# Kernel tuning notes

Hardware: AMD Instinct MI355X
Metric: run time of the kernel (lower is better)

Reference implementation:

```python
import jax, jax.numpy as jnp
import numpy as np
from jax import lax

M = 8   # num_heads
K = 4   # num_points


def conv2d(x, w, b, pad):
    # x: [B,C,H,W], w: [O,I,kh,kw]
    y = lax.conv_general_dilated(x, w, (1, 1), [(pad, pad), (pad, pad)],
                                 dimension_numbers=('NCHW', 'OIHW', 'NCHW'))
    return y + b[None, :, None, None]


def grid_sample_zeros(v, px, py):
    # Bilinear grid_sample, align_corners=True, padding_mode='zeros'.
    # v: [N,Cm,H,W]; px,py: [N,P] in pixel coordinates.
    N, Cm, H, W = v.shape
    x0 = jnp.floor(px); y0 = jnp.floor(py)
    x1 = x0 + 1.0;      y1 = y0 + 1.0
    wx = px - x0;       wy = py - y0
    vflat = v.reshape(N, Cm, H * W)

    def tap(xi, yi):
        valid = (xi >= 0) & (xi <= W - 1) & (yi >= 0) & (yi <= H - 1)
        xc = jnp.clip(xi, 0, W - 1).astype(jnp.int32)
        yc = jnp.clip(yi, 0, H - 1).astype(jnp.int32)
        idx = yc * W + xc                          # [N,P]
        g = jnp.take_along_axis(vflat, idx[:, None, :], axis=2)  # [N,Cm,P]
        return g * valid[:, None, :].astype(v.dtype)

    v00 = tap(x0, y0); v01 = tap(x1, y0)
    v10 = tap(x0, y1); v11 = tap(x1, y1)
    wx = wx[:, None, :]; wy = wy[:, None, :]
    return (v00 * (1 - wx) * (1 - wy) + v01 * wx * (1 - wy)
            + v10 * (1 - wx) * wy + v11 * wx * wy)


def setup_inputs() -> dict:
    key = jax.random.key(0)
    ks = jax.random.split(key, 16)
    B, C, H, W = 8, 256, 64, 64
    s = 0.02
    inp = {
        'f_recalib': jax.random.normal(ks[0], (B, C, H, W), jnp.float32),
        'f_orig':    jax.random.normal(ks[1], (B, C, H, W), jnp.float32),
        'offset_w': jax.random.normal(ks[2], (M * K * 2, C, 3, 3), jnp.float32) * s,
        'offset_b': jnp.zeros((M * K * 2,), jnp.float32),
        'attn_w':   jax.random.normal(ks[3], (M * K, C, 3, 3), jnp.float32) * s,
        'attn_b':   jnp.zeros((M * K,), jnp.float32),
        'value_w':  jax.random.normal(ks[4], (C, C, 1, 1), jnp.float32) * s,
        'value_b':  jnp.zeros((C,), jnp.float32),
        'proj_w':   jax.random.normal(ks[5], (C, C, 1, 1), jnp.float32) * s,
        'proj_b':   jnp.zeros((C,), jnp.float32),
        'mlp_w1':   jax.random.normal(ks[6], (2 * C, C, 1, 1), jnp.float32) * s,
        'mlp_b1':   jnp.zeros((2 * C,), jnp.float32),
        'mlp_w2':   jax.random.normal(ks[7], (C, 2 * C, 1, 1), jnp.float32) * s,
        'mlp_b2':   jnp.zeros((C,), jnp.float32),
    }
    return inp


def reference(f_recalib, f_orig, offset_w, offset_b, attn_w, attn_b,
              value_w, value_b, proj_w, proj_b,
              mlp_w1, mlp_b1, mlp_w2, mlp_b2):
    B, C, H, W = f_recalib.shape
    Cm = C // M

    offsets = conv2d(f_recalib, offset_w, offset_b, 1).reshape(B, M, K, 2, H, W)
    attn = conv2d(f_recalib, attn_w, attn_b, 1).reshape(B, M, K, H, W)
    attn = jax.nn.softmax(attn, axis=2)
    value = conv2d(f_recalib, value_w, value_b, 0)

    gy, gx = jnp.meshgrid(jnp.arange(H, dtype=jnp.float32),
                          jnp.arange(W, dtype=jnp.float32), indexing='ij')
    gx_sym = (W - 1) - gx  # horizontally mirrored x coordinate
    # pixel-space sampling locations (align_corners=True normalization is exactly
    # inverted by grid_sample's unnormalization, so work in pixel coords)
    px = gx_sym[None, None, None] + offsets[:, :, :, 0]  # [B,M,K,H,W]
    py = gy[None, None, None] + offsets[:, :, :, 1]

    v = value.reshape(B * M, Cm, H, W)
    sampled = grid_sample_zeros(v, px.reshape(B * M, -1), py.reshape(B * M, -1))
    sampled = sampled.reshape(B, M, Cm, K, H, W)

    out = (sampled * attn[:, :, None]).sum(axis=3).reshape(B, C, H, W)
    out = conv2d(out, proj_w, proj_b, 0) + f_orig
    h = jax.nn.relu(conv2d(out, mlp_w1, mlp_b1, 0))
    out = conv2d(h, mlp_w2, mlp_b2, 0) + out
    return out
```

## Files before the change

### kernel.cpp

```cpp
#include <hip/hip_runtime.h>
#include <cstddef>

#define P_ 4096
#define PW_ 66

using u16 = unsigned short;
typedef float  f32x4  __attribute__((ext_vector_type(4)));
typedef u16    u16x8  __attribute__((ext_vector_type(8)));
typedef u16    u16x4  __attribute__((ext_vector_type(4)));
typedef __bf16 bf16x8 __attribute__((ext_vector_type(8)));

#define DEVINL __device__ __forceinline__

DEVINL u16 f2bf(float f) {
    union { float f; unsigned u; } v; v.f = f;
    unsigned r = v.u + 0x7fffu + ((v.u >> 16) & 1u);
    return (u16)(r >> 16);
}
DEVINL float bf2f(u16 h) {
    union { unsigned u; float f; } v; v.u = ((unsigned)h) << 16;
    return v.f;
}

DEVINL f32x4 mfma16(u16x8 a, u16x8 b, f32x4 c) {
    return __builtin_amdgcn_mfma_f32_16x16x32_bf16(
        __builtin_bit_cast(bf16x8, a), __builtin_bit_cast(bf16x8, b), c, 0, 0, 0);
}

DEVINL void gload16(const u16* src, const u16* lds_dst) {
    __builtin_amdgcn_global_load_lds(
        (const __attribute__((address_space(1))) void*)src,
        (__attribute__((address_space(3))) void*)lds_dst, 16, 0, 0);
}

__global__ __launch_bounds__(256) void to_nhwc_pad(
    const float* __restrict__ in, u16* __restrict__ xp,
    const float* __restrict__ off_w, const float* __restrict__ attn_w,
    const float* __restrict__ val_w, const float* __restrict__ proj_w,
    const float* __restrict__ w1, const float* __restrict__ w2,
    u16* __restrict__ wbf) {
    const int bx = blockIdx.x, c0 = blockIdx.y * 64, b = blockIdx.z;
    const int t = threadIdx.x;

    if (bx >= 64) {
        const int idx = ((bx - 64) * 32 + blockIdx.y * 8 + b) * 256 + t;
        if (idx >= 614400) return;
        float v;
        if (idx < 221184) {
            int tap = idx / 24576, rem = idx - tap * 24576, oc = rem >> 8, ic = rem & 255;
            v = (oc < 64) ? off_w[(size_t)(oc * 256 + ic) * 9 + tap]
                          : attn_w[(size_t)((oc - 64) * 256 + ic) * 9 + tap];
        } else if (idx < 286720) v = val_w[idx - 221184];
        else if (idx < 352256)   v = proj_w[idx - 286720];
        else if (idx < 483328)   v = w1[idx - 352256];
        else                     v = w2[idx - 483328];
        wbf[idx] = f2bf(v);
        return;
    }

    const int y = bx;
    __shared__ u16 ts[64 * 72];
    const int cl = t >> 4, xq = t & 15;

    if (y == 0) {
        const u16x8 z = (u16x8){0, 0, 0, 0, 0, 0, 0, 0};
        for (int q = t; q < 2080; q += 256) {
            const int p = q >> 3, c8 = q & 7;
            int row, col;
            if (p < 66)       { row = 0;  col = p; }
            else if (p < 132) { row = 65; col = p - 66; }
            else { const int q2 = p - 132; row = 1 + (q2 >> 1); col = (q2 & 1) * 65; }
            *(u16x8*)&xp[((size_t)(b * PW_ + row) * PW_ + col) * 256 + c0 + c8 * 8] = z;
        }
    }

    #pragma unroll
    for (int r = 0; r < 4; ++r) {
        const int c = r * 16 + cl;
        const float4 v = *(const float4*)&in[((size_t)(b * 256 + c0 + c)) * P_ + y * 64 + xq * 4];
        ts[(xq * 4 + 0) * 72 + c] = f2bf(v.x);
        ts[(xq * 4 + 1) * 72 + c] = f2bf(v.y);
        ts[(xq * 4 + 2) * 72 + c] = f2bf(v.z);
        ts[(xq * 4 + 3) * 72 + c] = f2bf(v.w);
    }
    __syncthreads();
    const int px = t >> 2, seg = t & 3;
    u16x8 o0, o1;
    #pragma unroll
    for (int j = 0; j < 8; ++j) {
        o0[j] = ts[px * 72 + seg * 16 + j];
        o1[j] = ts[px * 72 + seg * 16 + 8 + j];
    }
    const size_t base = ((size_t)(b * PW_ + y + 1) * PW_ + 1 + px) * 256 + c0 + seg * 16;
    *(u16x8*)&xp[base]     = o0;
    *(u16x8*)&xp[base + 8] = o1;
}

__global__ __launch_bounds__(256, 2) void conv3x3_mfma(
    const u16* __restrict__ xp, const u16* __restrict__ wconv,
    const u16* __restrict__ wval,
    const float* __restrict__ off_b, const float* __restrict__ attn_b,
    const float* __restrict__ val_b,
    u16* __restrict__ convout, u16* __restrict__ value_bf) {
    const int y = blockIdx.x, b = blockIdx.y;
    const int tid = threadIdx.x, w = tid >> 6, lane = tid & 63, g = lane >> 4, i = lane & 15;
    const int wm = w & 1, wn = w >> 1;
    const int srow = lane >> 4, sc = lane & 15;
    __shared__ u16 lds[40960];

    f32x4 acc[2][3];
    #pragma unroll
    for (int mi = 0; mi < 2; ++mi)
        #pragma unroll
        for (int nj = 0; nj < 3; ++nj) acc[mi][nj] = (f32x4){0.f, 0.f, 0.f, 0.f};
    f32x4 accv[2][8];
    #pragma unroll
    for (int mi = 0; mi < 2; ++mi)
        #pragma unroll
        for (int nj = 0; nj < 8; ++nj) accv[mi][nj] = (f32x4){0.f, 0.f, 0.f, 0.f};

    auto stage = [&](int buf, int c) {
        const int tap = c >> 1, kc = (c & 1) * 128;
        const int dy = tap / 3, dx = tap % 3;
        const u16* xrow = xp + ((size_t)(b * PW_ + y + dy) * PW_ + dx) * 256;
        const u16* wt = wconv + (size_t)(tap * 96) * 256;
        u16* bufA = &lds[buf * 8192];
        u16* bufW = &lds[16384 + buf * 12288];
        #pragma unroll
        for (int t = 0; t < 4; ++t) {
            const int j = w * 4 + t;
            const int row = j * 4 + srow;
            const int cs = sc ^ (row & 7);
            gload16(xrow + (size_t)row * 256 + kc + (cs << 3), &bufA[j * 512]);
        }
        #pragma unroll
        for (int t = 0; t < 6; ++t) {
            const int j = w * 6 + t;
            const int row = j * 4 + srow;
            const int cs = sc ^ (row & 7);
            gload16(wt + (size_t)row * 256 + kc + (cs << 3), &bufW[j * 512]);
        }
    };

    stage(0, 0);
    stage(1, 1);
    asm volatile("s_waitcnt vmcnt(10)" ::: "memory");
    __builtin_amdgcn_s_barrier();

    for (int c = 0; c < 18; ++c) {
        const u16* bufA = &lds[(c & 1) * 8192];
        const u16* bufW = &lds[16384 + (c & 1) * 12288];
        const int kcv = (c & 1) * 128;
        const bool doval = (c == 8) | (c == 9);
        #pragma unroll
        for (int ks = 0; ks < 4; ++ks) {
            u16x8 a[2], bb[3];
            #pragma unroll
            for (int mi = 0; mi < 2; ++mi) {
                const int pr = wm * 32 + mi * 16 + i;
                a[mi] = *(const u16x8*)&bufA[pr * 128 + (((ks * 4 + g) ^ (pr & 7)) << 3)];
            }
            #pragma unroll
            for (int nj = 0; nj < 3; ++nj) {
                const int ocr = wn * 48 + nj * 16 + i;
                bb[nj] = *(const u16x8*)&bufW[ocr * 128 + (((ks * 4 + g) ^ (ocr & 7)) << 3)];
            }
            #pragma unroll
            for (int mi = 0; mi < 2; ++mi)
                #pragma unroll
                for (int nj = 0; nj < 3; ++nj)
                    acc[mi][nj] = mfma16(a[mi], bb[nj], acc[mi][nj]);
            if (doval) {
                #pragma unroll
                for (int nj = 0; nj < 8; ++nj) {
                    const int oc = wn * 128 + nj * 16 + i;
                    const u16x8 bv = *(const u16x8*)&wval[(size_t)oc * 256 + kcv
                                                          + ks * 32 + g * 8];
                    accv[0][nj] = mfma16(a[0], bv, accv[0][nj]);
                    accv[1][nj] = mfma16(a[1], bv, accv[1][nj]);
                }
            }
        }
        __builtin_amdgcn_sched_barrier(0);
        __builtin_amdgcn_s_barrier();
        if (c + 2 < 18) {
            stage(c & 1, c + 2);
            asm volatile("s_waitcnt vmcnt(10)" ::: "memory");
        } else {
            asm volatile("s_waitcnt vmcnt(0)" ::: "memory");
        }
        __builtin_amdgcn_s_barrier();
    }

    #pragma unroll
    for (int mi = 0; mi < 2; ++mi) {
        const int x0 = wm * 32 + mi * 16 + g * 4;
        #pragma unroll
        for (int nj = 0; nj < 3; ++nj) {
            const int oc = wn * 48 + nj * 16 + i;
            const float bv = (oc < 64) ? off_b[oc] : attn_b[oc - 64];
            #pragma unroll
            for (int r = 0; r < 4; ++r)
                convout[((size_t)(b * P_ + y * 64 + x0 + r)) * 96 + oc] =
                    f2bf(acc[mi][nj][r] + bv);
        }
        #pragma unroll
        for (int nj = 0; nj < 8; ++nj) {
            const int oc = wn * 128 + nj * 16 + i;
            const float bv = val_b[oc];
            #pragma unroll
            for (int r = 0; r < 4; ++r)
                value_bf[((size_t)(b * P_ + y * 64 + x0 + r)) * 256 + oc] =
                    f2bf(accv[mi][nj][r] + bv);
        }
    }
}

__global__ __launch_bounds__(256, 2) void gemm_dbuf(
    const u16* __restrict__ X, const u16* __restrict__ W,
    const float* __restrict__ bias, const void* __restrict__ resid,
    void* __restrict__ outA, u16* __restrict__ outB,
    const int KTOT, const int OC, const int mode) {
    const int px0 = blockIdx.x * 128, oc0 = blockIdx.y * 128, b = blockIdx.z;
    const int tid = threadIdx.x, w = tid >> 6, lane = tid & 63, g = lane >> 4, i = lane & 15;
    const int wm = w & 1, wn = w >> 1;
    __shared__ u16 lds[32768];
    u16* xs = lds;
    u16* wsL = lds + 16384;

    const int srcC = (lane & 7) ^ ((lane >> 3) & 7);

    f32x4 acc[4][4];
    #pragma unroll
    for (int mi = 0; mi < 4; ++mi)
        #pragma unroll
        for (int nj = 0; nj < 4; ++nj) acc[mi][nj] = (f32x4){0.f, 0.f, 0.f, 0.f};

    const int NC = KTOT >> 6;

    auto stage = [&](int buf, int kc) {
        #pragma unroll
        for (int t = 0; t < 4; ++t) {
            const int j = w * 4 + t;
            const int row = j * 8 + (lane >> 3);
            gload16(X + (size_t)(b * P_ + px0 + row) * KTOT + kc + (srcC << 3),
                    &xs[buf * 8192 + j * 512]);
        }
        #pragma unroll
        for (int t = 0; t < 4; ++t) {
            const int j = w * 4 + t;
            const int row = j * 8 + (lane >> 3);
            gload16(W + (size_t)(oc0 + row) * KTOT + kc + (srcC << 3),
                    &wsL[buf * 8192 + j * 512]);
        }
    };

    stage(0, 0);
    stage(1, 64);
    asm volatile("s_waitcnt vmcnt(8)" ::: "memory");
    __builtin_amdgcn_s_barrier();

    for (int c = 0; c < NC; ++c) {
        const u16* xb = &xs[(c & 1) * 8192];
        const u16* wb = &wsL[(c & 1) * 8192];
        #pragma unroll
        for (int ks = 0; ks < 2; ++ks) {
            u16x8 a[4], bb[4];
            #pragma unroll
            for (int mi = 0; mi < 4; ++mi) {
                const int row = wm * 64 + mi * 16 + i;
                a[mi] = *(const u16x8*)&xb[row * 64 + (((ks * 4 + g) ^ (row & 7)) << 3)];
            }
            #pragma unroll
            for (int nj = 0; nj < 4; ++nj) {
                const int row = wn * 64 + nj * 16 + i;
                bb[nj] = *(const u16x8*)&wb[row * 64 + (((ks * 4 + g) ^ (row & 7)) << 3)];
            }
            #pragma unroll
            for (int mi = 0; mi < 4; ++mi)
                #pragma unroll
                for (int nj = 0; nj < 4; ++nj)
                    acc[mi][nj] = mfma16(a[mi], bb[nj], acc[mi][nj]);
        }
        __builtin_amdgcn_sched_barrier(0);
        __builtin_amdgcn_s_barrier();
        if (c + 2 < NC) {
            stage(c & 1, (c + 2) << 6);
            asm volatile("s_waitcnt vmcnt(8)" ::: "memory");
        } else {
            asm volatile("s_waitcnt vmcnt(0)" ::: "memory");
        }
        __builtin_amdgcn_s_barrier();
    }

    float* lf = (float*)lds;
    const int pxq = tid >> 2, segq = tid & 3;
    const int oclh = tid >> 1, shh = (tid & 1) * 32;

    #pragma unroll
    for (int h = 0; h < 2; ++h) {
        if (wm == h) {
            #pragma unroll
            for (int nj = 0; nj < 4; ++nj) {
                const int ocl = wn * 64 + nj * 16 + i;
                const float bv = bias[oc0 + ocl];
                #pragma unroll
                for (int mi = 0; mi < 4; ++mi)
                    #pragma unroll
                    for (int r = 0; r < 4; ++r)
                        lf[ocl * 66 + mi * 16 + g * 4 + r] = acc[mi][nj][r] + bv;
            }
        }
        __syncthreads();
        const int pxg0 = px0 + h * 64;

        if (mode == 4) {
            const float* rf = (const float*)resid;
            const size_t rb = ((size_t)b * 256 + oc0 + oclh) * P_ + pxg0 + shh;
            #pragma unroll
            for (int q = 0; q < 8; ++q) {
                const float4 r4 = *(const float4*)&rf[rb + q * 4];
                lf[oclh * 66 + shh + q * 4 + 0] += r4.x;
                lf[oclh * 66 + shh + q * 4 + 1] += r4.y;
                lf[oclh * 66 + shh + q * 4 + 2] += r4.z;
                lf[oclh * 66 + shh + q * 4 + 3] += r4.w;
            }
            __syncthreads();
        }
        if (mode == 6) {
            const u16* rn = (const u16*)resid;
            const size_t nb = ((size_t)(b * P_ + pxg0 + pxq)) * 256 + oc0 + segq * 32;
            #pragma unroll
            for (int t2 = 0; t2 < 4; ++t2) {
                const u16x8 r8 = *(const u16x8*)&rn[nb + t2 * 8];
                #pragma unroll
                for (int jj = 0; jj < 8; ++jj)
                    lf[(segq * 32 + t2 * 8 + jj) * 66 + pxq] += bf2f(r8[jj]);
            }
            __syncthreads();
        }

        if (mode <= 1 || mode == 4) {
            const size_t nb = ((size_t)(b * P_ + pxg0 + pxq)) * OC + oc0 + segq * 32;
            #pragma unroll
            for (int t2 = 0; t2 < 4; ++t2) {
                u16x8 o8;
                #pragma unroll
                for (int jj = 0; jj < 8; ++jj) {
                    float v = lf[(segq * 32 + t2 * 8 + jj) * 66 + pxq];
                    if (mode == 1) v = fmaxf(v, 0.f);
                    o8[jj] = f2bf(v);
                }
                *(u16x8*)&outB[nb + t2 * 8] = o8;
            }
        }
        if (mode == 6) {
            float* of = (float*)outA;
            const size_t cb = ((size_t)b * 256 + oc0 + oclh) * P_ + pxg0 + shh;
            #pragma unroll
            for (int q = 0; q < 8; ++q) {
                float4 o;
                o.x = lf[oclh * 66 + shh + q * 4 + 0];
                o.y = lf[oclh * 66 + shh + q * 4 + 1];
                o.z = lf[oclh * 66 + shh + q * 4 + 2];
                o.w = lf[oclh * 66 + shh + q * 4 + 3];
                *(float4*)&of[cb + q * 4] = o;
            }
        }
        __syncthreads();
    }
}

__global__ __launch_bounds__(256) void sample_attend_bf(
    const u16* __restrict__ value, const u16* __restrict__ conv,
    u16* __restrict__ out1) {
    const int y = blockIdx.x, m = blockIdx.y, b = blockIdx.z;
    const int tid = threadIdx.x, x = tid >> 2, gq = tid & 3;
    const int w = tid >> 6, lane = tid & 63;
    const int wlo = max(0, y - 3), whi = min(63, y + 4);
    const int nchunks = (whi - wlo + 1) * 256;
    __shared__ u16 vlds[8 * 64 * 32];

    const u16* vbase = value + ((size_t)b * P_) * 256 + m * 32;
    for (int it = w; it * 64 < nchunks; it += 4) {
        const int cid = it * 64 + lane;
        const int r = cid >> 8, px = (cid >> 2) & 63, cc = cid & 3;
        gload16(vbase + ((size_t)((wlo + r) * 64 + px)) * 256 + cc * 8,
                &vlds[it * 512]);
    }

    const size_t prow = (size_t)(b * P_ + y * 64 + x);
    const u16x8 ov = *(const u16x8*)&conv[prow * 96 + m * 8];
    const u16x4 av = *(const u16x4*)&conv[prow * 96 + 64 + m * 4];
    float a[4];
    #pragma unroll
    for (int k = 0; k < 4; ++k) a[k] = bf2f(av[k]);
    const float mx = fmaxf(fmaxf(a[0], a[1]), fmaxf(a[2], a[3]));
    float s = 0.f;
    #pragma unroll
    for (int k = 0; k < 4; ++k) { a[k] = __expf(a[k] - mx); s += a[k]; }
    const float inv = 1.f / s;

    __syncthreads();

    float acc[8];
    #pragma unroll
    for (int j = 0; j < 8; ++j) acc[j] = 0.f;

    #pragma unroll
    for (int k = 0; k < 4; ++k) {
        const float offx = bf2f(ov[2 * k]), offy = bf2f(ov[2 * k + 1]);
        const float px = (float)(63 - x) + offx;
        const float py = (float)y + offy;
        const float x0f = floorf(px), y0f = floorf(py);
        const int xi0 = (int)x0f, yi0 = (int)y0f;
        const float wx = px - x0f, wy = py - y0f;
        const int xi1 = xi0 + 1, yi1 = yi0 + 1;
        const bool vx0 = (xi0 >= 0) & (xi0 <= 63), vx1 = (xi1 >= 0) & (xi1 <= 63);
        const bool vy0 = (yi0 >= 0) & (yi0 <= 63), vy1 = (yi1 >= 0) & (yi1 <= 63);
        const int cx0 = min(max(xi0, 0), 63), cx1 = min(max(xi1, 0), 63);
        const int cy0 = min(max(yi0, 0), 63), cy1 = min(max(yi1, 0), 63);
        const float ak = a[k] * inv;
        const float c00 = ak * (1.f - wx) * (1.f - wy) * ((vx0 & vy0) ? 1.f : 0.f);
        const float c01 = ak * wx * (1.f - wy) * ((vx1 & vy0) ? 1.f : 0.f);
        const float c10 = ak * (1.f - wx) * wy * ((vx0 & vy1) ? 1.f : 0.f);
        const float c11 = ak * wx * wy * ((vx1 & vy1) ? 1.f : 0.f);
        u16x8 v00, v01, v10, v11;
        const bool inWin = (cy0 >= wlo) & (cy1 <= whi);
        if (inWin) {
            const int r0 = (cy0 - wlo) * 64, r1 = (cy1 - wlo) * 64;
            v00 = *(const u16x8*)&vlds[(r0 + cx0) * 32 + gq * 8];
            v01 = *(const u16x8*)&vlds[(r0 + cx1) * 32 + gq * 8];
            v10 = *(const u16x8*)&vlds[(r1 + cx0) * 32 + gq * 8];
            v11 = *(const u16x8*)&vlds[(r1 + cx1) * 32 + gq * 8];
        } else {
            const u16* vb = vbase + gq * 8;
            v00 = *(const u16x8*)&vb[(size_t)(cy0 * 64 + cx0) * 256];
            v01 = *(const u16x8*)&vb[(size_t)(cy0 * 64 + cx1) * 256];
            v10 = *(const u16x8*)&vb[(size_t)(cy1 * 64 + cx0) * 256];
            v11 = *(const u16x8*)&vb[(size_t)(cy1 * 64 + cx1) * 256];
        }
        #pragma unroll
        for (int j = 0; j < 8; ++j)
            acc[j] += c00 * bf2f(v00[j]) + c01 * bf2f(v01[j])
                    + c10 * bf2f(v10[j]) + c11 * bf2f(v11[j]);
    }
    u16x8 o;
    #pragma unroll
    for (int j = 0; j < 8; ++j) o[j] = f2bf(acc[j]);
    *(u16x8*)&out1[prow * 256 + m * 32 + gq * 8] = o;
}

extern "C" void kernel_launch(void* const* d_in, const int* in_sizes, int n_in,
                              void* d_out, int out_size, void* d_ws, size_t ws_size,
                              hipStream_t stream) {
    const float* f_recalib = (const float*)d_in[0];
    const float* f_orig    = (const float*)d_in[1];
    const float* offset_w  = (const float*)d_in[2];
    const float* offset_b  = (const float*)d_in[3];
    const float* attn_w    = (const float*)d_in[4];
    const float* attn_b    = (const float*)d_in[5];
    const float* value_w   = (const float*)d_in[6];
    const float* value_b   = (const float*)d_in[7];
    const float* proj_w    = (const float*)d_in[8];
    const float* proj_b    = (const float*)d_in[9];
    const float* mlp_w1    = (const float*)d_in[10];
    const float* mlp_b1    = (const float*)d_in[11];
    const float* mlp_w2    = (const float*)d_in[12];
    const float* mlp_b2    = (const float*)d_in[13];
    float* out = (float*)d_out;

    u16* wsb       = (u16*)d_ws;
    u16* x_pad     = wsb;
    u16* convout   = wsb + 8921088;
    u16* value_bf  = wsb + 12066816;
    u16* out1_bf   = wsb + 20455424;
    u16* wbf       = wsb + 28844032;
    u16* out2_bf   = x_pad;
    u16* h_bf      = wsb + 8921088;

    u16* wconv = wbf;
    u16* wval  = wbf + 221184;
    u16* wproj = wbf + 286720;
    u16* wmlp1 = wbf + 352256;
    u16* wmlp2 = wbf + 483328;

    to_nhwc_pad<<<dim3(139, 4, 8), 256, 0, stream>>>(
        f_recalib, x_pad, offset_w, attn_w, value_w, proj_w, mlp_w1, mlp_w2, wbf);
    conv3x3_mfma<<<dim3(64, 8), 256, 0, stream>>>(
        x_pad, wconv, wval, offset_b, attn_b, value_b, convout, value_bf);
    sample_attend_bf<<<dim3(64, 8, 8), 256, 0, stream>>>(value_bf, convout, out1_bf);
    gemm_dbuf<<<dim3(32, 2, 8), 256, 0, stream>>>(out1_bf, wproj, proj_b, f_orig,
                                                  nullptr, out2_bf, 256, 256, 4);
    gemm_dbuf<<<dim3(32, 4, 8), 256, 0, stream>>>(out2_bf, wmlp1, mlp_b1, nullptr,
                                                  nullptr, h_bf, 256, 512, 1);
    gemm_dbuf<<<dim3(32, 2, 8), 256, 0, stream>>>(h_bf, wmlp2, mlp_b2, out2_bf,
                                                  out, nullptr, 512, 256, 6);
}
```

Before: 144.4 us.

## Split value 1x1 GEMM into separate interleaved blocks alongside 3x3 conv

Previously each conv block also computed the value projection during the center-tap iterations, which serialized extra MFMAs and uncached global weight loads into one block. Now the grid has 1024 blocks alternating between conv3x3 work (offset/attn) and a standalone double-buffered 128x128 value GEMM with LDS-staged weights and a coalesced transposed store. This spreads work across more blocks for better CU utilization, at the cost of re-reading the center-tap input for the value path.

```diff
diff --git a/kernel.cpp b/kernel.cpp
--- a/kernel.cpp
+++ b/kernel.cpp
@@ -96,122 +96,200 @@
     *(u16x8*)&xp[base + 8] = o1;
 }
 
-__global__ __launch_bounds__(256, 2) void conv3x3_mfma(
+__global__ __launch_bounds__(256, 2) void conv_value(
     const u16* __restrict__ xp, const u16* __restrict__ wconv,
     const u16* __restrict__ wval,
     const float* __restrict__ off_b, const float* __restrict__ attn_b,
     const float* __restrict__ val_b,
     u16* __restrict__ convout, u16* __restrict__ value_bf) {
-    const int y = blockIdx.x, b = blockIdx.y;
+    const int bid = blockIdx.x;
+    const int id = bid >> 1;
     const int tid = threadIdx.x, w = tid >> 6, lane = tid & 63, g = lane >> 4, i = lane & 15;
     const int wm = w & 1, wn = w >> 1;
-    const int srow = lane >> 4, sc = lane & 15;
     __shared__ u16 lds[40960];
 
-    f32x4 acc[2][3];
-    #pragma unroll
-    for (int mi = 0; mi < 2; ++mi)
-        #pragma unroll
-        for (int nj = 0; nj < 3; ++nj) acc[mi][nj] = (f32x4){0.f, 0.f, 0.f, 0.f};
-    f32x4 accv[2][8];
-    #pragma unroll
-    for (int mi = 0; mi < 2; ++mi)
-        #pragma unroll
-        for (int nj = 0; nj < 8; ++nj) accv[mi][nj] = (f32x4){0.f, 0.f, 0.f, 0.f};
-
-    auto stage = [&](int buf, int c) {
-        const int tap = c >> 1, kc = (c & 1) * 128;
-        const int dy = tap / 3, dx = tap % 3;
-        const u16* xrow = xp + ((size_t)(b * PW_ + y + dy) * PW_ + dx) * 256;
-        const u16* wt = wconv + (size_t)(tap * 96) * 256;
-        u16* bufA = &lds[buf * 8192];
-        u16* bufW = &lds[16384 + buf * 12288];
-        #pragma unroll
-        for (int t = 0; t < 4; ++t) {
-            const int j = w * 4 + t;
-            const int row = j * 4 + srow;
-            const int cs = sc ^ (row & 7);
-            gload16(xrow + (size_t)row * 256 + kc + (cs << 3), &bufA[j * 512]);
-        }
-        #pragma unroll
-        for (int t = 0; t < 6; ++t) {
-            const int j = w * 6 + t;
-            const int row = j * 4 + srow;
-            const int cs = sc ^ (row & 7);
-            gload16(wt + (size_t)row * 256 + kc + (cs << 3), &bufW[j * 512]);
-        }
-    };
-
-    stage(0, 0);
-    stage(1, 1);
-    asm volatile("s_waitcnt vmcnt(10)" ::: "memory");
-    __builtin_amdgcn_s_barrier();
-
-    for (int c = 0; c < 18; ++c) {
-        const u16* bufA = &lds[(c & 1) * 8192];
-        const u16* bufW = &lds[16384 + (c & 1) * 12288];
-        const int kcv = (c & 1) * 128;
-        const bool doval = (c == 8) | (c == 9);
-        #pragma unroll
-        for (int ks = 0; ks < 4; ++ks) {
-            u16x8 a[2], bb[3];
-            #pragma unroll
-            for (int mi = 0; mi < 2; ++mi) {
-                const int pr = wm * 32 + mi * 16 + i;
-                a[mi] = *(const u16x8*)&bufA[pr * 128 + (((ks * 4 + g) ^ (pr & 7)) << 3)];
-            }
+    if ((bid & 1) == 0) {
+        const int y = id & 63, b = id >> 6;
+        const int srow = lane >> 4, sc = lane & 15;
+
+        f32x4 acc[2][3];
+        #pragma unroll
+        for (int mi = 0; mi < 2; ++mi)
+            #pragma unroll
+            for (int nj = 0; nj < 3; ++nj) acc[mi][nj] = (f32x4){0.f, 0.f, 0.f, 0.f};
+
+        auto stage = [&](int buf, int c) {
+            const int tap = c >> 1, kc = (c & 1) * 128;
+            const int dy = tap / 3, dx = tap % 3;
+            const u16* xrow = xp + ((size_t)(b * PW_ + y + dy) * PW_ + dx) * 256;
+            const u16* wt = wconv + (size_t)(tap * 96) * 256;
+            u16* bufA = &lds[buf * 8192];
+            u16* bufW = &lds[16384 + buf * 12288];
+            #pragma unroll
+            for (int t = 0; t < 4; ++t) {
+                const int j = w * 4 + t;
+                const int row = j * 4 + srow;
+                const int cs = sc ^ (row & 7);
+                gload16(xrow + (size_t)row * 256 + kc + (cs << 3), &bufA[j * 512]);
+            }
+            #pragma unroll
+            for (int t = 0; t < 6; ++t) {
+                const int j = w * 6 + t;
+                const int row = j * 4 + srow;
+                const int cs = sc ^ (row & 7);
+                gload16(wt + (size_t)row * 256 + kc + (cs << 3), &bufW[j * 512]);
+            }
+        };
+
+        stage(0, 0);
+        stage(1, 1);
+        asm volatile("s_waitcnt vmcnt(10)" ::: "memory");
+        __builtin_amdgcn_s_barrier();
+
+        for (int c = 0; c < 18; ++c) {
+            const u16* bufA = &lds[(c & 1) * 8192];
+            const u16* bufW = &lds[16384 + (c & 1) * 12288];
+            #pragma unroll
+            for (int ks = 0; ks < 4; ++ks) {
+                u16x8 a[2], bb[3];
+                #pragma unroll
+                for (int mi = 0; mi < 2; ++mi) {
+                    const int pr = wm * 32 + mi * 16 + i;
+                    a[mi] = *(const u16x8*)&bufA[pr * 128 + (((ks * 4 + g) ^ (pr & 7)) << 3)];
+                }
+                #pragma unroll
+                for (int nj = 0; nj < 3; ++nj) {
+                    const int ocr = wn * 48 + nj * 16 + i;
+                    bb[nj] = *(const u16x8*)&bufW[ocr * 128 + (((ks * 4 + g) ^ (ocr & 7)) << 3)];
+                }
+                #pragma unroll
+                for (int mi = 0; mi < 2; ++mi)
+                    #pragma unroll
+                    for (int nj = 0; nj < 3; ++nj)
+                        acc[mi][nj] = mfma16(a[mi], bb[nj], acc[mi][nj]);
+            }
+            __builtin_amdgcn_sched_barrier(0);
+            __builtin_amdgcn_s_barrier();
+            if (c + 2 < 18) {
+                stage(c & 1, c + 2);
+                asm volatile("s_waitcnt vmcnt(10)" ::: "memory");
+            } else {
+                asm volatile("s_waitcnt vmcnt(0)" ::: "memory");
+            }
+            __builtin_amdgcn_s_barrier();
+        }
+
+        #pragma unroll
+        for (int mi = 0; mi < 2; ++mi) {
+            const int x0 = wm * 32 + mi * 16 + g * 4;
             #pragma unroll
             for (int nj = 0; nj < 3; ++nj) {
-                const int ocr = wn * 48 + nj * 16 + i;
-                bb[nj] = *(const u16x8*)&bufW[ocr * 128 + (((ks * 4 + g) ^ (ocr & 7)) << 3)];
-            }
-            #pragma unroll
-            for (int mi = 0; mi < 2; ++mi)
-                #pragma unroll
-                for (int nj = 0; nj < 3; ++nj)
-                    acc[mi][nj] = mfma16(a[mi], bb[nj], acc[mi][nj]);
-            if (doval) {
-                #pragma unroll
-                for (int nj = 0; nj < 8; ++nj) {
-                    const int oc = wn * 128 + nj * 16 + i;
-                    const u16x8 bv = *(const u16x8*)&wval[(size_t)oc * 256 + kcv
-                                                          + ks * 32 + g * 8];
-                    accv[0][nj] = mfma16(a[0], bv, accv[0][nj]);
-                    accv[1][nj] = mfma16(a[1], bv, accv[1][nj]);
+                const int oc = wn * 48 + nj * 16 + i;
+                const float bv = (oc < 64) ? off_b[oc] : attn_b[oc - 64];
+                #pragma unroll
+                for (int r = 0; r < 4; ++r)
+                    convout[((size_t)(b * P_ + y * 64 + x0 + r)) * 96 + oc] =
+                        f2bf(acc[mi][nj][r] + bv);
+            }
+        }
+    } else {
+        const int px0 = (id & 31) * 128, oc0 = ((id >> 5) & 1) * 128, b = id >> 6;
+        u16* xs = lds;
+        u16* wsL = lds + 16384;
+        const int srcC = (lane & 7) ^ ((lane >> 3) & 7);
+
+        f32x4 acc[4][4];
+        #pragma unroll
+        for (int mi = 0; mi < 4; ++mi)
+            #pragma unroll
+            for (int nj = 0; nj < 4; ++nj) acc[mi][nj] = (f32x4){0.f, 0.f, 0.f, 0.f};
+
+        auto stage = [&](int buf, int kc) {
+            #pragma unroll
+            for (int t = 0; t < 4; ++t) {
+                const int j = w * 4 + t;
+                const int row = j * 8 + (lane >> 3);
+                const int pxg = px0 + row;
+                gload16(xp + ((size_t)(b * PW_ + (pxg >> 6) + 1) * PW_ + (pxg & 63) + 1) * 256
+                           + kc + (srcC << 3),
+                        &xs[buf * 8192 + j * 512]);
+            }
+            #pragma unroll
+            for (int t = 0; t < 4; ++t) {
+                const int j = w * 4 + t;
+                const int row = j * 8 + (lane >> 3);
+                gload16(wval + (size_t)(oc0 + row) * 256 + kc + (srcC << 3),
+                        &wsL[buf * 8192 + j * 512]);
+            }
+        };
+
+        stage(0, 0);
+        stage(1, 64);
+        asm volatile("s_waitcnt vmcnt(8)" ::: "memory");
+        __builtin_amdgcn_s_barrier();
+
+        for (int c = 0; c < 4; ++c) {
+            const u16* xb = &xs[(c & 1) * 8192];
+            const u16* wb = &wsL[(c & 1) * 8192];
+            #pragma unroll
+            for (int ks = 0; ks < 2; ++ks) {
+                u16x8 a[4], bb[4];
+                #pragma unroll
+                for (int mi = 0; mi < 4; ++mi) {
+                    const int row = wm * 64 + mi * 16 + i;
+                    a[mi] = *(const u16x8*)&xb[row * 64 + (((ks * 4 + g) ^ (row & 7)) << 3)];
                 }
-            }
-        }
-        __builtin_amdgcn_sched_barrier(0);
-        __builtin_amdgcn_s_barrier();
-        if (c + 2 < 18) {
-            stage(c & 1, c + 2);
-            asm volatile("s_waitcnt vmcnt(10)" ::: "memory");
-        } else {
-            asm volatile("s_waitcnt vmcnt(0)" ::: "memory");
-        }
-        __builtin_amdgcn_s_barrier();
-    }
-
-    #pragma unroll
-    for (int mi = 0; mi < 2; ++mi) {
-        const int x0 = wm * 32 + mi * 16 + g * 4;
-        #pragma unroll
-        for (int nj = 0; nj < 3; ++nj) {
-            const int oc = wn * 48 + nj * 16 + i;
-            const float bv = (oc < 64) ? off_b[oc] : attn_b[oc - 64];
-            #pragma unroll
-            for (int r = 0; r < 4; ++r)
-                convout[((size_t)(b * P_ + y * 64 + x0 + r)) * 96 + oc] =
-                    f2bf(acc[mi][nj][r] + bv);
-        }
-        #pragma unroll
-        for (int nj = 0; nj < 8; ++nj) {
-            const int oc = wn * 128 + nj * 16 + i;
-            const float bv = val_b[oc];
-            #pragma unroll
-            for (int r = 0; r < 4; ++r)
-                value_bf[((size_t)(b * P_ + y * 64 + x0 + r)) * 256 + oc] =
-                    f2bf(accv[mi][nj][r] + bv);
+                #pragma unroll
+                for (int nj = 0; nj < 4; ++nj) {
+                    const int row = wn * 64 + nj * 16 + i;
+                    bb[nj] = *(const u16x8*)&wb[row * 64 + (((ks * 4 + g) ^ (row & 7)) << 3)];
+                }
+                #pragma unroll
+                for (int mi = 0; mi < 4; ++mi)
+                    #pragma unroll
+                    for (int nj = 0; nj < 4; ++nj)
+                        acc[mi][nj] = mfma16(a[mi], bb[nj], acc[mi][nj]);
+            }
+            __builtin_amdgcn_sched_barrier(0);
+            __builtin_amdgcn_s_barrier();
+            if (c + 2 < 4) {
+                stage(c & 1, (c + 2) << 6);
+                asm volatile("s_waitcnt vmcnt(8)" ::: "memory");
+            } else {
+                asm volatile("s_waitcnt vmcnt(0)" ::: "memory");
+            }
+            __builtin_amdgcn_s_barrier();
+        }
+
+        float* lf = (float*)lds;
+        const int pxq = tid >> 2, segq = tid & 3;
+
+        #pragma unroll
+        for (int h = 0; h < 2; ++h) {
+            if (wm == h) {
+                #pragma unroll
+                for (int nj = 0; nj < 4; ++nj) {
+                    const int ocl = wn * 64 + nj * 16 + i;
+                    const float bv = val_b[oc0 + ocl];
+                    #pragma unroll
+                    for (int mi = 0; mi < 4; ++mi)
+                        #pragma unroll
+                        for (int r = 0; r < 4; ++r)
+                            lf[ocl * 66 + mi * 16 + g * 4 + r] = acc[mi][nj][r] + bv;
+                }
+            }
+            __syncthreads();
+            const int pxg0 = px0 + h * 64;
+            const size_t nb = ((size_t)(b * P_ + pxg0 + pxq)) * 256 + oc0 + segq * 32;
+            #pragma unroll
+            for (int t2 = 0; t2 < 4; ++t2) {
+                u16x8 o8;
+                #pragma unroll
+                for (int jj = 0; jj < 8; ++jj)
+                    o8[jj] = f2bf(lf[(segq * 32 + t2 * 8 + jj) * 66 + pxq]);
+                *(u16x8*)&value_bf[nb + t2 * 8] = o8;
+            }
+            __syncthreads();
         }
     }
 }
@@ -487,7 +565,7 @@
 
     to_nhwc_pad<<<dim3(139, 4, 8), 256, 0, stream>>>(
         f_recalib, x_pad, offset_w, attn_w, value_w, proj_w, mlp_w1, mlp_w2, wbf);
-    conv3x3_mfma<<<dim3(64, 8), 256, 0, stream>>>(
+    conv_value<<<dim3(1024), 256, 0, stream>>>(
         x_pad, wconv, wval, offset_b, attn_b, value_b, convout, value_bf);
     sample_attend_bf<<<dim3(64, 8, 8), 256, 0, stream>>>(value_bf, convout, out1_bf);
     gemm_dbuf<<<dim3(32, 2, 8), 256, 0, stream>>>(out1_bf, wproj, proj_b, f_orig,
```

Result: no change. 143.7 us, median of 2 (-0.5%).
